# Kernel optimization log

Hardware: AMD Instinct MI355X
Metric: run time of the kernel (lower is better)

The kernel has to match this reference:

```python
import jax, jax.numpy as jnp
import numpy as np

M = 0.4        # margin
H = 0.333      # margin scaler slope
S = 64.0       # logit scale
BN_MEAN = 20.0     # running_mean of norm normalizer (affine=False, eval stats)
BN_VAR = 100.0 * 100.0
BN_EPS = 1e-3


def setup_inputs() -> dict:
    key = jax.random.key(0)
    k1, k2, k3 = jax.random.split(key, 3)
    embs = jax.random.normal(k1, (1024, 512), dtype=jnp.float32)
    weight = jax.random.normal(k2, (100000, 512), dtype=jnp.float32)
    labels = jax.random.randint(k3, (1024,), 0, 100000)
    return {"embs": embs, "weight": weight, "labels": labels}


def reference(embs, weight, labels):
    n = embs.shape[0]
    rows = jnp.arange(n)
    # feature norms and cosine logits
    norms = jnp.linalg.norm(embs, axis=1, keepdims=True)            # [N,1]
    w_norm = weight / jnp.linalg.norm(weight, axis=1, keepdims=True)  # [C,D]
    logits = (embs / norms) @ w_norm.T                               # [N,C]
    # norm-adaptive margin scaler (BatchNorm1d with running stats, affine=False)
    g = (norms[:, 0] - BN_MEAN) / jnp.sqrt(BN_VAR + BN_EPS)
    g = jnp.clip(g * H, -1.0, 1.0)                                   # [N]
    # angular margin at the label position
    theta = jnp.arccos(jnp.clip(logits.astype(jnp.float32), -0.999, 0.999))
    theta = theta.at[rows, labels].add(-M * g)
    logits_m = jnp.cos(jnp.clip(theta, 0.0, jnp.pi))
    # additive margin at the label position
    logits_m = logits_m.at[rows, labels].add(-(1.0 + M) * g)
    # scaled softmax cross-entropy (mean over batch)
    logp = jax.nn.log_softmax(logits_m * S, axis=-1)
    return -jnp.mean(logp[rows, labels])
```

## Files before the change

### kernel.cpp

```cpp
#include <hip/hip_runtime.h>
#include <math.h>

constexpr int N_ROWS = 1024;
constexpr int DDIM   = 512;
constexpr int C_CLS  = 100000;
constexpr float MARG = 0.4f;
constexpr int WPAD   = 100352;
constexpr int NT2    = 392;
constexpr int NT_FB  = 782;

typedef __attribute__((ext_vector_type(8))) short bf16x8;
typedef __attribute__((ext_vector_type(4))) float f32x4;
typedef __attribute__((address_space(1))) const void gvoid_t;
typedef __attribute__((address_space(3))) void lvoid_t;

__device__ __forceinline__ unsigned int f2bf(float x) {
    union { float f; unsigned int u; } v; v.f = x;
    return (v.u + 0x7FFFu + ((v.u >> 16) & 1u)) >> 16;
}

__device__ __forceinline__ float wave_sum(float s) {
    #pragma unroll
    for (int m = 1; m < 64; m <<= 1) s += __shfl_xor(s, m, 64);
    return s;
}

__global__ __launch_bounds__(256) void prep_embs(const float* __restrict__ embs,
                                                 float* __restrict__ g,
                                                 unsigned short* __restrict__ ehat) {
    const int row  = blockIdx.x * 4 + (threadIdx.x >> 6);
    const int lane = threadIdx.x & 63;
    const float4* src = (const float4*)(embs + (size_t)row * DDIM + lane * 8);
    const float4 a = src[0], b = src[1];
    float ss = a.x*a.x + a.y*a.y + a.z*a.z + a.w*a.w
             + b.x*b.x + b.y*b.y + b.z*b.z + b.w*b.w;
    ss = wave_sum(ss);
    const float norm = sqrtf(ss);
    const float rn = 1.f / norm;
    if (lane == 0) {
        float gg = (norm - 20.f) / sqrtf(10000.f + 1e-3f) * 0.333f;
        gg = fminf(fmaxf(gg, -1.f), 1.f);
        g[row] = gg;
    }
    uint4 pk;
    pk.x = f2bf(a.x*rn) | (f2bf(a.y*rn) << 16);
    pk.y = f2bf(a.z*rn) | (f2bf(a.w*rn) << 16);
    pk.z = f2bf(b.x*rn) | (f2bf(b.y*rn) << 16);
    pk.w = f2bf(b.z*rn) | (f2bf(b.w*rn) << 16);
    *(uint4*)(ehat + (size_t)row * DDIM + lane * 8) = pk;
}

__global__ __launch_bounds__(256) void prep_what(const float* __restrict__ w,
                                                 unsigned short* __restrict__ what) {
    const int row  = blockIdx.x * 4 + (threadIdx.x >> 6);
    const int lane = threadIdx.x & 63;
    const float4* src = (const float4*)(w + (size_t)row * DDIM + lane * 8);
    const float4 a = src[0], b = src[1];
    float ss = a.x*a.x + a.y*a.y + a.z*a.z + a.w*a.w
             + b.x*b.x + b.y*b.y + b.z*b.z + b.w*b.w;
    ss = wave_sum(ss);
    const float rn = rsqrtf(ss);
    uint4 pk;
    pk.x = f2bf(a.x*rn) | (f2bf(a.y*rn) << 16);
    pk.y = f2bf(a.z*rn) | (f2bf(a.w*rn) << 16);
    pk.z = f2bf(b.x*rn) | (f2bf(b.y*rn) << 16);
    pk.w = f2bf(b.z*rn) | (f2bf(b.w*rn) << 16);
    *(uint4*)(what + (size_t)row * DDIM + lane * 8) = pk;
}

__global__ __launch_bounds__(256) void prep_wnorm(const float* __restrict__ w,
                                                  float* __restrict__ rnormw) {
    const int row  = blockIdx.x * 4 + (threadIdx.x >> 6);
    const int lane = threadIdx.x & 63;
    const float4* src = (const float4*)(w + (size_t)row * DDIM + lane * 8);
    const float4 a = src[0], b = src[1];
    float ss = a.x*a.x + a.y*a.y + a.z*a.z + a.w*a.w
             + b.x*b.x + b.y*b.y + b.z*b.z + b.w*b.w;
    ss = wave_sum(ss);
    if (lane == 0) rnormw[row] = 1.f / sqrtf(ss);
}

__device__ __forceinline__ void stage_slab(const unsigned short* __restrict__ src,
                                           int grow0, const unsigned short* lds_row0,
                                           int kbase, int lane) {
    const int lr  = lane >> 3;
    const int c16 = (lane & 7) ^ lr;
    const unsigned short* g = src + (size_t)(grow0 + lr) * DDIM + kbase + c16 * 8;
    __builtin_amdgcn_global_load_lds((gvoid_t*)g, (lvoid_t*)lds_row0, 16, 0, 0);
}
__device__ __forceinline__ bf16x8 frag_ld(const unsigned short* tile, int row, int ks, int lane) {
    const int c16 = ((ks << 2) + (lane >> 4)) ^ (lane & 7);
    return *(const bf16x8*)(tile + row * 64 + c16 * 8);
}

__global__ __launch_bounds__(512, 2) void gemm256(
        const unsigned short* __restrict__ ehat,
        const unsigned short* __restrict__ what,
        const int* __restrict__ labels,
        float* __restrict__ psum,
        float* __restrict__ dlab)
{
    __shared__ __align__(16) unsigned short As[2][256 * 64];
    __shared__ __align__(16) unsigned short Bs[2][256 * 64];

    const int tid  = threadIdx.x;
    const int lane = tid & 63;
    const int wv   = tid >> 6;
    const int wr   = wv >> 2;
    const int wc   = wv & 3;

    const int nchunk = (int)gridDim.x >> 3;
    const int wgid   = ((int)blockIdx.x & 7) * nchunk + ((int)blockIdx.x >> 3);
    const int tile_c = wgid >> 2;
    const int tile_r = wgid & 3;
    const int row0   = tile_r * 256;
    const int col0   = tile_c * 256;

    f32x4 acc[8][4];
    #pragma unroll
    for (int m = 0; m < 8; ++m)
        #pragma unroll
        for (int n = 0; n < 4; ++n) acc[m][n] = f32x4{0.f, 0.f, 0.f, 0.f};

    #pragma unroll
    for (int s = 0; s < 8; ++s) {
        const int base = (s & 3) * 64 + wv * 8;
        if (s < 4) stage_slab(ehat, row0 + base, &As[0][base * 64], 0, lane);
        else       stage_slab(what, col0 + base, &Bs[0][base * 64], 0, lane);
    }
    asm volatile("s_waitcnt vmcnt(0)" ::: "memory");
    __builtin_amdgcn_s_barrier();

    for (int h = 0; h < 8; ++h) {
        const int cur = h & 1;
        const unsigned short* At = As[cur];
        const unsigned short* Bt = Bs[cur];
        const unsigned short* An = As[cur ^ 1];
        const unsigned short* Bn = Bs[cur ^ 1];
        const int kn = (h + 1) * 64;
        const bool do_stage = (h < 7);

        bf16x8 af[4][2], bf[4][2];

        #pragma unroll
        for (int q = 0; q < 4; ++q) {
            const int mh = q >> 1, nh = q & 1;
            if (q == 0 || q == 2) {
                #pragma unroll
                for (int m = 0; m < 4; ++m)
                    #pragma unroll
                    for (int ks = 0; ks < 2; ++ks)
                        af[m][ks] = frag_ld(At, wr * 128 + (mh * 4 + m) * 16 + (lane & 15), ks, lane);
            }
            if (q == 0 || q == 1) {
                #pragma unroll
                for (int n = 0; n < 2; ++n)
                    #pragma unroll
                    for (int ks = 0; ks < 2; ++ks)
                        bf[nh * 2 + n][ks] = frag_ld(Bt, wc * 64 + (nh * 2 + n) * 16 + (lane & 15), ks, lane);
            }
            if (do_stage) {
                #pragma unroll
                for (int s = 0; s < 8; ++s) {
                    const bool mine = (q == 0) ? (s < 3) : (q == 1) ? (s >= 3 && s < 6)
                                    : (q == 2) ? (s >= 6) : false;
                    if (mine) {
                        const int base = (s & 3) * 64 + wv * 8;
                        if (s < 4) stage_slab(ehat, row0 + base, &An[base * 64], kn, lane);
                        else       stage_slab(what, col0 + base, &Bn[base * 64], kn, lane);
                    }
                }
            }
            __builtin_amdgcn_s_barrier();
            asm volatile("s_waitcnt lgkmcnt(0)" ::: "memory");
            __builtin_amdgcn_s_setprio(1);
            #pragma unroll
            for (int m = 0; m < 4; ++m)
                #pragma unroll
                for (int n = 0; n < 2; ++n)
                    #pragma unroll
                    for (int ks = 0; ks < 2; ++ks)
                        acc[mh * 4 + m][nh * 2 + n] =
                            __builtin_amdgcn_mfma_f32_16x16x32_bf16(af[m][ks], bf[nh * 2 + n][ks],
                                                                    acc[mh * 4 + m][nh * 2 + n], 0, 0, 0);
            __builtin_amdgcn_s_setprio(0);
            if (q == 3) asm volatile("s_waitcnt vmcnt(0)" ::: "memory");
            __builtin_amdgcn_s_barrier();
        }
    }

    float* red = (float*)&As[0][0];
    #pragma unroll
    for (int m = 0; m < 8; ++m) {
        #pragma unroll
        for (int j = 0; j < 4; ++j) {
            const int lrow  = wr * 128 + m * 16 + ((lane >> 4) << 2) + j;
            const int r_abs = row0 + lrow;
            const int lab   = labels[r_abs];
            float s = 0.f;
            #pragma unroll
            for (int n = 0; n < 4; ++n) {
                const int c_abs = col0 + wc * 64 + n * 16 + (lane & 15);
                float v = acc[m][n][j];
                v = fminf(fmaxf(v, -0.999f), 0.999f);
                if (c_abs == lab) dlab[r_abs] = v;
                if (c_abs < C_CLS) s += __expf(64.f * v - 64.f);
            }
            #pragma unroll
            for (int msk = 1; msk < 16; msk <<= 1) s += __shfl_xor(s, msk, 64);
            if ((lane & 15) == 0) red[wc * 256 + lrow] = s;
        }
    }
    __syncthreads();
    for (int t = tid; t < 256; t += 512)
        psum[(size_t)(row0 + t) * NT2 + tile_c] = red[t] + red[256 + t] + red[512 + t] + red[768 + t];
}

__global__ __launch_bounds__(256, 2) void gemm_fused_fb(
        const unsigned short* __restrict__ ehat,
        const float* __restrict__ weight,
        const float* __restrict__ rnormw,
        const int* __restrict__ labels,
        float* __restrict__ psum,
        float* __restrict__ dlab)
{
    constexpr int BM = 128, BN = 128, BK = 32;
    __shared__ __align__(16) unsigned short Asf[BM * BK];
    __shared__ __align__(16) unsigned short Bsf[BN * BK];
    __shared__ float redbuf[2][BM];

    const int bid    = blockIdx.x;
    const int tile_c = bid >> 3;
    const int tile_r = bid & 7;
    const int row0   = tile_r * BM;
    const int col0   = tile_c * BN;

    const int tid  = threadIdx.x;
    const int lane = tid & 63;
    const int wv   = tid >> 6;
    const int wr   = wv >> 1;
    const int wc   = wv & 1;

    f32x4 acc[4][4];
    #pragma unroll
    for (int m = 0; m < 4; ++m)
        #pragma unroll
        for (int n = 0; n < 4; ++n) acc[m][n] = f32x4{0.f, 0.f, 0.f, 0.f};

    const int kq    = tid & 7;
    const int brow0 = tid >> 3;
    int   cidx[4];
    float rnv[4];
    #pragma unroll
    for (int p = 0; p < 4; ++p) {
        int c = col0 + p * 32 + brow0;
        c = c < C_CLS ? c : C_CLS - 1;
        cidx[p] = c;
        rnv[p]  = rnormw[c];
    }

    for (int kt = 0; kt < DDIM / BK; ++kt) {
        const int kbase = kt * BK;
        #pragma unroll
        for (int call = 0; call < 2; ++call) {
            const int chunk = call * 256 + tid;
            const uint4 d = *(const uint4*)(ehat + (size_t)(row0 + (chunk >> 2)) * DDIM
                                            + kbase + (chunk & 3) * 8);
            *(uint4*)(Asf + chunk * 8) = d;
        }
        #pragma unroll
        for (int p = 0; p < 4; ++p) {
            const float4 wd = *(const float4*)(weight + (size_t)cidx[p] * DDIM + kbase + kq * 4);
            const float r = rnv[p];
            const unsigned int lo = f2bf(wd.x * r) | (f2bf(wd.y * r) << 16);
            const unsigned int hi = f2bf(wd.z * r) | (f2bf(wd.w * r) << 16);
            *(uint2*)(Bsf + (p * 32 + brow0) * BK + kq * 4) = make_uint2(lo, hi);
        }
        __syncthreads();
        bf16x8 af[4], bfr[4];
        const int lr  = lane & 15;
        const int lko = (lane >> 4) * 8;
        #pragma unroll
        for (int m = 0; m < 4; ++m)
            af[m] = *(const bf16x8*)(Asf + (wr * 64 + m * 16 + lr) * BK + lko);
        #pragma unroll
        for (int n = 0; n < 4; ++n)
            bfr[n] = *(const bf16x8*)(Bsf + (wc * 64 + n * 16 + lr) * BK + lko);
        #pragma unroll
        for (int m = 0; m < 4; ++m)
            #pragma unroll
            for (int n = 0; n < 4; ++n)
                acc[m][n] = __builtin_amdgcn_mfma_f32_16x16x32_bf16(af[m], bfr[n], acc[m][n], 0, 0, 0);
        __syncthreads();
    }

    #pragma unroll
    for (int m = 0; m < 4; ++m) {
        #pragma unroll
        for (int j = 0; j < 4; ++j) {
            const int lrow  = wr * 64 + m * 16 + ((lane >> 4) << 2) + j;
            const int r_abs = row0 + lrow;
            const int lab   = labels[r_abs];
            float s = 0.f;
            #pragma unroll
            for (int n = 0; n < 4; ++n) {
                const int c_abs = col0 + wc * 64 + n * 16 + (lane & 15);
                float v = acc[m][n][j];
                v = fminf(fmaxf(v, -0.999f), 0.999f);
                if (c_abs == lab) dlab[r_abs] = v;
                if (c_abs < C_CLS) s += __expf(64.f * v - 64.f);
            }
            #pragma unroll
            for (int msk = 1; msk < 16; msk <<= 1) s += __shfl_xor(s, msk, 64);
            if ((lane & 15) == 0) redbuf[wc][lrow] = s;
        }
    }
    __syncthreads();
    for (int t = tid; t < BM; t += 256)
        psum[(size_t)(row0 + t) * NT_FB + tile_c] = redbuf[0][t] + redbuf[1][t];
}

__global__ __launch_bounds__(256) void reduce_rows(const float* __restrict__ psum,
                                                   const float* __restrict__ dlab,
                                                   const float* __restrict__ g,
                                                   float* __restrict__ losses, int nt) {
    const int row  = blockIdx.x * 4 + (threadIdx.x >> 6);
    const int lane = threadIdx.x & 63;
    const float* p = psum + (size_t)row * nt;
    float s = 0.f;
    for (int t = lane; t < nt; t += 64) s += p[t];
    s = wave_sum(s);
    if (lane == 0) {
        const float v  = dlab[row];
        const float gg = g[row];
        float th = acosf(v) - MARG * gg;
        th = fminf(fmaxf(th, 0.f), 3.14159265358979323846f);
        const float vm = cosf(th) - (1.f + MARG) * gg;
        s = s - __expf(64.f * v - 64.f) + __expf(64.f * vm - 64.f);
        losses[row] = 64.f + logf(s) - 64.f * vm;
    }
}

__global__ __launch_bounds__(256) void final_mean(const float* __restrict__ losses,
                                                  float* __restrict__ out) {
    const int tid = threadIdx.x;
    float s = 0.f;
    #pragma unroll
    for (int i = 0; i < 4; ++i) s += losses[tid + i * 256];
    s = wave_sum(s);
    __shared__ float red[4];
    if ((tid & 63) == 0) red[tid >> 6] = s;
    __syncthreads();
    if (tid == 0) out[0] = (red[0] + red[1] + red[2] + red[3]) * (1.f / 1024.f);
}

extern "C" void kernel_launch(void* const* d_in, const int* in_sizes, int n_in,
                              void* d_out, int out_size, void* d_ws, size_t ws_size,
                              hipStream_t stream) {
    const float* embs   = (const float*)d_in[0];
    const float* weight = (const float*)d_in[1];
    const int*   labels = (const int*)d_in[2];
    float* out = (float*)d_out;
    float* ws  = (float*)d_ws;

    const size_t WHAT_F = (size_t)WPAD * DDIM / 2;
    const size_t EHAT_F = (size_t)N_ROWS * DDIM / 2;
    const size_t PSUM_F = (size_t)N_ROWS * NT2;
    const size_t NEED_F = WHAT_F + EHAT_F + PSUM_F + 3 * 1024;

    if (ws_size >= NEED_F * sizeof(float)) {
        unsigned short* what = (unsigned short*)ws;
        unsigned short* ehat = (unsigned short*)(ws + WHAT_F);
        float* psum   = ws + WHAT_F + EHAT_F;
        float* gbuf   = psum + PSUM_F;
        float* dlab   = gbuf + 1024;
        float* losses = dlab + 1024;

        prep_embs<<<N_ROWS / 4, 256, 0, stream>>>(embs, gbuf, ehat);
        prep_what<<<C_CLS / 4, 256, 0, stream>>>(weight, what);
        gemm256<<<NT2 * 4, 512, 0, stream>>>(ehat, what, labels, psum, dlab);
        reduce_rows<<<N_ROWS / 4, 256, 0, stream>>>(psum, dlab, gbuf, losses, NT2);
        final_mean<<<1, 256, 0, stream>>>(losses, out);
    } else {
        float* rnormw = ws + 0;
        float* gbuf   = ws + 100352;
        float* dlab   = ws + 101376;
        float* losses = ws + 102400;
        unsigned short* ehat = (unsigned short*)(ws + 103424);
        float* psum   = ws + 103424 + 262144;

        prep_embs <<<N_ROWS / 4, 256, 0, stream>>>(embs, gbuf, ehat);
        prep_wnorm<<<C_CLS / 4, 256, 0, stream>>>(weight, rnormw);
        gemm_fused_fb<<<NT_FB * 8, 256, 0, stream>>>(ehat, weight, rnormw, labels, psum, dlab);
        reduce_rows<<<N_ROWS / 4, 256, 0, stream>>>(psum, dlab, gbuf, losses, NT_FB);
        final_mean<<<1, 256, 0, stream>>>(losses, out);
    }
}
```

Measured before the change: 222.6 us.

## Replace double-buffered K=64 GEMM pipeline with 4-slot K=32 ring prefetching three ahead

```diff
diff --git a/kernel.cpp b/kernel.cpp
--- a/kernel.cpp
+++ b/kernel.cpp
@@ -8,6 +8,7 @@
 constexpr int WPAD   = 100352;
 constexpr int NT2    = 392;
 constexpr int NT_FB  = 782;
+constexpr int TSLOT  = 256 * 32;
 
 typedef __attribute__((ext_vector_type(8))) short bf16x8;
 typedef __attribute__((ext_vector_type(4))) float f32x4;
@@ -80,28 +81,32 @@
     if (lane == 0) rnormw[row] = 1.f / sqrtf(ss);
 }
 
-__device__ __forceinline__ void stage_slab(const unsigned short* __restrict__ src,
-                                           int grow0, const unsigned short* lds_row0,
-                                           int kbase, int lane) {
-    const int lr  = lane >> 3;
-    const int c16 = (lane & 7) ^ lr;
-    const unsigned short* g = src + (size_t)(grow0 + lr) * DDIM + kbase + c16 * 8;
-    __builtin_amdgcn_global_load_lds((gvoid_t*)g, (lvoid_t*)lds_row0, 16, 0, 0);
-}
-__device__ __forceinline__ bf16x8 frag_ld(const unsigned short* tile, int row, int ks, int lane) {
-    const int c16 = ((ks << 2) + (lane >> 4)) ^ (lane & 7);
-    return *(const bf16x8*)(tile + row * 64 + c16 * 8);
-}
-
-__global__ __launch_bounds__(512, 2) void gemm256(
+__device__ __forceinline__ void stage_tile(const unsigned short* __restrict__ src,
+                                           int grow0, unsigned short* tile,
+                                           int kbase, int tid, int wv) {
+    #pragma unroll
+    for (int i = 0; i < 2; ++i) {
+        const int r  = i * 128 + (tid >> 2);
+        const int lc = (tid & 3) ^ ((r >> 1) & 3);
+        const unsigned short* g = src + (size_t)(grow0 + r) * DDIM + kbase + lc * 8;
+        __builtin_amdgcn_global_load_lds((gvoid_t*)g,
+            (lvoid_t*)(tile + i * 4096 + wv * 512), 16, 0, 0);
+    }
+}
+__device__ __forceinline__ bf16x8 frag32(const unsigned short* tile, int row, int lane) {
+    const int pc = (lane >> 4) ^ ((row >> 1) & 3);
+    return *(const bf16x8*)(tile + row * 32 + pc * 8);
+}
+
+__global__ __launch_bounds__(512, 2) void gemm256p(
         const unsigned short* __restrict__ ehat,
         const unsigned short* __restrict__ what,
         const int* __restrict__ labels,
         float* __restrict__ psum,
         float* __restrict__ dlab)
 {
-    __shared__ __align__(16) unsigned short As[2][256 * 64];
-    __shared__ __align__(16) unsigned short Bs[2][256 * 64];
+    __shared__ __align__(16) unsigned short Abuf[4 * TSLOT];
+    __shared__ __align__(16) unsigned short Bbuf[4 * TSLOT];
 
     const int tid  = threadIdx.x;
     const int lane = tid & 63;
@@ -123,73 +128,51 @@
         for (int n = 0; n < 4; ++n) acc[m][n] = f32x4{0.f, 0.f, 0.f, 0.f};
 
     #pragma unroll
-    for (int s = 0; s < 8; ++s) {
-        const int base = (s & 3) * 64 + wv * 8;
-        if (s < 4) stage_slab(ehat, row0 + base, &As[0][base * 64], 0, lane);
-        else       stage_slab(what, col0 + base, &Bs[0][base * 64], 0, lane);
-    }
+    for (int t = 0; t < 3; ++t) {
+        stage_tile(ehat, row0, Abuf + t * TSLOT, t * 32, tid, wv);
+        stage_tile(what, col0, Bbuf + t * TSLOT, t * 32, tid, wv);
+    }
+    asm volatile("s_waitcnt vmcnt(8)" ::: "memory");
+    __builtin_amdgcn_s_barrier();
+
+    auto body = [&](int h, bool do_stage) {
+        if (do_stage) {
+            const int hn = h + 3;
+            stage_tile(ehat, row0, Abuf + (hn & 3) * TSLOT, hn * 32, tid, wv);
+            stage_tile(what, col0, Bbuf + (hn & 3) * TSLOT, hn * 32, tid, wv);
+        }
+        const unsigned short* At = Abuf + (h & 3) * TSLOT;
+        const unsigned short* Bt = Bbuf + (h & 3) * TSLOT;
+        bf16x8 af[8], bf[4];
+        #pragma unroll
+        for (int m = 0; m < 8; ++m)
+            af[m] = frag32(At, wr * 128 + m * 16 + (lane & 15), lane);
+        #pragma unroll
+        for (int n = 0; n < 4; ++n)
+            bf[n] = frag32(Bt, wc * 64 + n * 16 + (lane & 15), lane);
+        __builtin_amdgcn_s_setprio(1);
+        #pragma unroll
+        for (int m = 0; m < 8; ++m)
+            #pragma unroll
+            for (int n = 0; n < 4; ++n)
+                acc[m][n] = __builtin_amdgcn_mfma_f32_16x16x32_bf16(af[m], bf[n], acc[m][n], 0, 0, 0);
+        __builtin_amdgcn_s_setprio(0);
+    };
+
+    for (int h = 0; h < 13; ++h) {
+        body(h, true);
+        asm volatile("s_waitcnt vmcnt(8)" ::: "memory");
+        __builtin_amdgcn_s_barrier();
+    }
+    body(13, false);
+    asm volatile("s_waitcnt vmcnt(4)" ::: "memory");
+    __builtin_amdgcn_s_barrier();
+    body(14, false);
     asm volatile("s_waitcnt vmcnt(0)" ::: "memory");
     __builtin_amdgcn_s_barrier();
-
-    for (int h = 0; h < 8; ++h) {
-        const int cur = h & 1;
-        const unsigned short* At = As[cur];
-        const unsigned short* Bt = Bs[cur];
-        const unsigned short* An = As[cur ^ 1];
-        const unsigned short* Bn = Bs[cur ^ 1];
-        const int kn = (h + 1) * 64;
-        const bool do_stage = (h < 7);
-
-        bf16x8 af[4][2], bf[4][2];
-
-        #pragma unroll
-        for (int q = 0; q < 4; ++q) {
-            const int mh = q >> 1, nh = q & 1;
-            if (q == 0 || q == 2) {
-                #pragma unroll
-                for (int m = 0; m < 4; ++m)
-                    #pragma unroll
-                    for (int ks = 0; ks < 2; ++ks)
-                        af[m][ks] = frag_ld(At, wr * 128 + (mh * 4 + m) * 16 + (lane & 15), ks, lane);
-            }
-            if (q == 0 || q == 1) {
-                #pragma unroll
-                for (int n = 0; n < 2; ++n)
-                    #pragma unroll
-                    for (int ks = 0; ks < 2; ++ks)
-                        bf[nh * 2 + n][ks] = frag_ld(Bt, wc * 64 + (nh * 2 + n) * 16 + (lane & 15), ks, lane);
-            }
-            if (do_stage) {
-                #pragma unroll
-                for (int s = 0; s < 8; ++s) {
-                    const bool mine = (q == 0) ? (s < 3) : (q == 1) ? (s >= 3 && s < 6)
-                                    : (q == 2) ? (s >= 6) : false;
-                    if (mine) {
-                        const int base = (s & 3) * 64 + wv * 8;
-                        if (s < 4) stage_slab(ehat, row0 + base, &An[base * 64], kn, lane);
-                        else       stage_slab(what, col0 + base, &Bn[base * 64], kn, lane);
-                    }
-                }
-            }
-            __builtin_amdgcn_s_barrier();
-            asm volatile("s_waitcnt lgkmcnt(0)" ::: "memory");
-            __builtin_amdgcn_s_setprio(1);
-            #pragma unroll
-            for (int m = 0; m < 4; ++m)
-                #pragma unroll
-                for (int n = 0; n < 2; ++n)
-                    #pragma unroll
-                    for (int ks = 0; ks < 2; ++ks)
-                        acc[mh * 4 + m][nh * 2 + n] =
-                            __builtin_amdgcn_mfma_f32_16x16x32_bf16(af[m][ks], bf[nh * 2 + n][ks],
-                                                                    acc[mh * 4 + m][nh * 2 + n], 0, 0, 0);
-            __builtin_amdgcn_s_setprio(0);
-            if (q == 3) asm volatile("s_waitcnt vmcnt(0)" ::: "memory");
-            __builtin_amdgcn_s_barrier();
-        }
-    }
-
-    float* red = (float*)&As[0][0];
+    body(15, false);
+
+    float* red = (float*)&Abuf[0];
     #pragma unroll
     for (int m = 0; m < 8; ++m) {
         #pragma unroll
@@ -378,7 +361,7 @@
 
         prep_embs<<<N_ROWS / 4, 256, 0, stream>>>(embs, gbuf, ehat);
         prep_what<<<C_CLS / 4, 256, 0, stream>>>(weight, what);
-        gemm256<<<NT2 * 4, 512, 0, stream>>>(ehat, what, labels, psum, dlab);
+        gemm256p<<<NT2 * 4, 512, 0, stream>>>(ehat, what, labels, psum, dlab);
         reduce_rows<<<N_ROWS / 4, 256, 0, stream>>>(psum, dlab, gbuf, losses, NT2);
         final_mean<<<1, 256, 0, stream>>>(losses, out);
     } else {
```

Result: no change. 222.6 us (+0.0%).

## Split LDS tiles into halves and prefetch halves across quadrant phases

Applied to the files above, without the earlier changes.

```diff
diff --git a/kernel.cpp b/kernel.cpp
--- a/kernel.cpp
+++ b/kernel.cpp
@@ -8,11 +8,14 @@
 constexpr int WPAD   = 100352;
 constexpr int NT2    = 392;
 constexpr int NT_FB  = 782;
+constexpr int TILE   = 256 * 64;
 
 typedef __attribute__((ext_vector_type(8))) short bf16x8;
 typedef __attribute__((ext_vector_type(4))) float f32x4;
 typedef __attribute__((address_space(1))) const void gvoid_t;
 typedef __attribute__((address_space(3))) void lvoid_t;
+
+#define WAITV(N) asm volatile("s_waitcnt vmcnt(" #N ")" ::: "memory")
 
 __device__ __forceinline__ unsigned int f2bf(float x) {
     union { float f; unsigned int u; } v; v.f = x;
@@ -80,34 +83,53 @@
     if (lane == 0) rnormw[row] = 1.f / sqrtf(ss);
 }
 
-__device__ __forceinline__ void stage_slab(const unsigned short* __restrict__ src,
-                                           int grow0, const unsigned short* lds_row0,
-                                           int kbase, int lane) {
-    const int lr  = lane >> 3;
-    const int c16 = (lane & 7) ^ lr;
-    const unsigned short* g = src + (size_t)(grow0 + lr) * DDIM + kbase + c16 * 8;
-    __builtin_amdgcn_global_load_lds((gvoid_t*)g, (lvoid_t*)lds_row0, 16, 0, 0);
-}
-__device__ __forceinline__ bf16x8 frag_ld(const unsigned short* tile, int row, int ks, int lane) {
-    const int c16 = ((ks << 2) + (lane >> 4)) ^ (lane & 7);
-    return *(const bf16x8*)(tile + row * 64 + c16 * 8);
-}
-
-__global__ __launch_bounds__(512, 2) void gemm256(
+__device__ __forceinline__ void stageA(const unsigned short* __restrict__ src, int grow0,
+                                       unsigned short* tile, int g, int kbase,
+                                       int wv, int lane) {
+    const int lr = lane >> 3;
+    const int lc = (lane & 7) ^ lr;
+    #pragma unroll
+    for (int i = 0; i < 2; ++i) {
+        const int s  = i * 8 + wv;
+        const int rb = ((s >> 3) << 7) | (g << 6) | ((s & 7) << 3);
+        const unsigned short* gp = src + (size_t)(grow0 + rb + lr) * DDIM + kbase + lc * 8;
+        __builtin_amdgcn_global_load_lds((gvoid_t*)gp, (lvoid_t*)(tile + rb * 64), 16, 0, 0);
+    }
+}
+__device__ __forceinline__ void stageB(const unsigned short* __restrict__ src, int grow0,
+                                       unsigned short* tile, int g, int kbase,
+                                       int wv, int lane) {
+    const int lr = lane >> 3;
+    const int lc = (lane & 7) ^ lr;
+    #pragma unroll
+    for (int i = 0; i < 2; ++i) {
+        const int s  = i * 8 + wv;
+        const int rb = ((s >> 2) << 6) | (g << 5) | ((s & 3) << 3);
+        const unsigned short* gp = src + (size_t)(grow0 + rb + lr) * DDIM + kbase + lc * 8;
+        __builtin_amdgcn_global_load_lds((gvoid_t*)gp, (lvoid_t*)(tile + rb * 64), 16, 0, 0);
+    }
+}
+__device__ __forceinline__ bf16x8 frag64(const unsigned short* tile, int row, int ks, int lane) {
+    const int pc = ((ks << 2) + (lane >> 4)) ^ (lane & 7);
+    return *(const bf16x8*)(tile + row * 64 + pc * 8);
+}
+
+__global__ __launch_bounds__(512, 2) void gemm256q(
         const unsigned short* __restrict__ ehat,
         const unsigned short* __restrict__ what,
         const int* __restrict__ labels,
         float* __restrict__ psum,
         float* __restrict__ dlab)
 {
-    __shared__ __align__(16) unsigned short As[2][256 * 64];
-    __shared__ __align__(16) unsigned short Bs[2][256 * 64];
+    __shared__ __align__(16) unsigned short Abuf[2 * TILE];
+    __shared__ __align__(16) unsigned short Bbuf[2 * TILE];
 
     const int tid  = threadIdx.x;
     const int lane = tid & 63;
     const int wv   = tid >> 6;
     const int wr   = wv >> 2;
     const int wc   = wv & 3;
+    const int lr15 = lane & 15;
 
     const int nchunk = (int)gridDim.x >> 3;
     const int wgid   = ((int)blockIdx.x & 7) * nchunk + ((int)blockIdx.x >> 3);
@@ -122,74 +144,108 @@
         #pragma unroll
         for (int n = 0; n < 4; ++n) acc[m][n] = f32x4{0.f, 0.f, 0.f, 0.f};
 
-    #pragma unroll
-    for (int s = 0; s < 8; ++s) {
-        const int base = (s & 3) * 64 + wv * 8;
-        if (s < 4) stage_slab(ehat, row0 + base, &As[0][base * 64], 0, lane);
-        else       stage_slab(what, col0 + base, &Bs[0][base * 64], 0, lane);
-    }
-    asm volatile("s_waitcnt vmcnt(0)" ::: "memory");
+    stageA(ehat, row0, Abuf, 0, 0, wv, lane);
+    stageB(what, col0, Bbuf, 0, 0, wv, lane);
+    stageA(ehat, row0, Abuf, 1, 0, wv, lane);
+    stageB(what, col0, Bbuf, 1, 0, wv, lane);
+    stageA(ehat, row0, Abuf + TILE, 0, 64, wv, lane);
+    stageB(what, col0, Bbuf + TILE, 0, 64, wv, lane);
+    WAITV(8);
     __builtin_amdgcn_s_barrier();
 
-    for (int h = 0; h < 8; ++h) {
-        const int cur = h & 1;
-        const unsigned short* At = As[cur];
-        const unsigned short* Bt = Bs[cur];
-        const unsigned short* An = As[cur ^ 1];
-        const unsigned short* Bn = Bs[cur ^ 1];
-        const int kn = (h + 1) * 64;
-        const bool do_stage = (h < 7);
-
-        bf16x8 af[4][2], bf[4][2];
-
-        #pragma unroll
-        for (int q = 0; q < 4; ++q) {
-            const int mh = q >> 1, nh = q & 1;
-            if (q == 0 || q == 2) {
+    for (int t = 0; t < 8; ++t) {
+        unsigned short* curA = Abuf + (t & 1) * TILE;
+        unsigned short* curB = Bbuf + (t & 1) * TILE;
+        unsigned short* nxtA = Abuf + ((t & 1) ^ 1) * TILE;
+        unsigned short* nxtB = Bbuf + ((t & 1) ^ 1) * TILE;
+        bf16x8 af[4][2], bfv[2][2][2];
+
+        #pragma unroll
+        for (int m = 0; m < 4; ++m)
+            #pragma unroll
+            for (int ks = 0; ks < 2; ++ks)
+                af[m][ks] = frag64(curA, wr * 128 + m * 16 + lr15, ks, lane);
+        #pragma unroll
+        for (int n = 0; n < 2; ++n)
+            #pragma unroll
+            for (int ks = 0; ks < 2; ++ks)
+                bfv[0][n][ks] = frag64(curB, wc * 64 + n * 16 + lr15, ks, lane);
+        if (t < 7) stageA(ehat, row0, nxtA, 1, (t + 1) * 64, wv, lane);
+        __builtin_amdgcn_sched_barrier(0);
+        __builtin_amdgcn_s_barrier();
+        asm volatile("s_waitcnt lgkmcnt(0)" ::: "memory");
+        __builtin_amdgcn_sched_barrier(0);
+        __builtin_amdgcn_s_setprio(1);
+        #pragma unroll
+        for (int m = 0; m < 4; ++m)
+            #pragma unroll
+            for (int n = 0; n < 2; ++n)
                 #pragma unroll
-                for (int m = 0; m < 4; ++m)
-                    #pragma unroll
-                    for (int ks = 0; ks < 2; ++ks)
-                        af[m][ks] = frag_ld(At, wr * 128 + (mh * 4 + m) * 16 + (lane & 15), ks, lane);
-            }
-            if (q == 0 || q == 1) {
+                for (int ks = 0; ks < 2; ++ks)
+                    acc[m][n] = __builtin_amdgcn_mfma_f32_16x16x32_bf16(af[m][ks], bfv[0][n][ks], acc[m][n], 0, 0, 0);
+        __builtin_amdgcn_s_setprio(0);
+        if (t < 7) { WAITV(6); } else { WAITV(0); }
+        __builtin_amdgcn_s_barrier();
+
+        #pragma unroll
+        for (int n = 0; n < 2; ++n)
+            #pragma unroll
+            for (int ks = 0; ks < 2; ++ks)
+                bfv[1][n][ks] = frag64(curB, wc * 64 + 32 + n * 16 + lr15, ks, lane);
+        if (t < 7) stageB(what, col0, nxtB, 1, (t + 1) * 64, wv, lane);
+        __builtin_amdgcn_sched_barrier(0);
+        __builtin_amdgcn_s_barrier();
+        asm volatile("s_waitcnt lgkmcnt(0)" ::: "memory");
+        __builtin_amdgcn_sched_barrier(0);
+        __builtin_amdgcn_s_setprio(1);
+        #pragma unroll
+        for (int m = 0; m < 4; ++m)
+            #pragma unroll
+            for (int n = 0; n < 2; ++n)
                 #pragma unroll
-                for (int n = 0; n < 2; ++n)
-                    #pragma unroll
-                    for (int ks = 0; ks < 2; ++ks)
-                        bf[nh * 2 + n][ks] = frag_ld(Bt, wc * 64 + (nh * 2 + n) * 16 + (lane & 15), ks, lane);
-            }
-            if (do_stage) {
+                for (int ks = 0; ks < 2; ++ks)
+                    acc[m][2 + n] = __builtin_amdgcn_mfma_f32_16x16x32_bf16(af[m][ks], bfv[1][n][ks], acc[m][2 + n], 0, 0, 0);
+        __builtin_amdgcn_s_setprio(0);
+        __builtin_amdgcn_s_barrier();
+
+        #pragma unroll
+        for (int m = 0; m < 4; ++m)
+            #pragma unroll
+            for (int ks = 0; ks < 2; ++ks)
+                af[m][ks] = frag64(curA, wr * 128 + 64 + m * 16 + lr15, ks, lane);
+        if (t < 6) stageA(ehat, row0, curA, 0, (t + 2) * 64, wv, lane);
+        __builtin_amdgcn_sched_barrier(0);
+        __builtin_amdgcn_s_barrier();
+        asm volatile("s_waitcnt lgkmcnt(0)" ::: "memory");
+        __builtin_amdgcn_sched_barrier(0);
+        __builtin_amdgcn_s_setprio(1);
+        #pragma unroll
+        for (int m = 0; m < 4; ++m)
+            #pragma unroll
+            for (int n = 0; n < 2; ++n)
                 #pragma unroll
-                for (int s = 0; s < 8; ++s) {
-                    const bool mine = (q == 0) ? (s < 3) : (q == 1) ? (s >= 3 && s < 6)
-                                    : (q == 2) ? (s >= 6) : false;
-                    if (mine) {
-                        const int base = (s & 3) * 64 + wv * 8;
-                        if (s < 4) stage_slab(ehat, row0 + base, &An[base * 64], kn, lane);
-                        else       stage_slab(what, col0 + base, &Bn[base * 64], kn, lane);
-                    }
-                }
-            }
-            __builtin_amdgcn_s_barrier();
-            asm volatile("s_waitcnt lgkmcnt(0)" ::: "memory");
-            __builtin_amdgcn_s_setprio(1);
-            #pragma unroll
-            for (int m = 0; m < 4; ++m)
+                for (int ks = 0; ks < 2; ++ks)
+                    acc[4 + m][n] = __builtin_amdgcn_mfma_f32_16x16x32_bf16(af[m][ks], bfv[0][n][ks], acc[4 + m][n], 0, 0, 0);
+        __builtin_amdgcn_s_setprio(0);
+        __builtin_amdgcn_s_barrier();
+
+        if (t < 6) stageB(what, col0, curB, 0, (t + 2) * 64, wv, lane);
+        __builtin_amdgcn_sched_barrier(0);
+        __builtin_amdgcn_s_barrier();
+        __builtin_amdgcn_s_setprio(1);
+        #pragma unroll
+        for (int m = 0; m < 4; ++m)
+            #pragma unroll
+            for (int n = 0; n < 2; ++n)
                 #pragma unroll
-                for (int n = 0; n < 2; ++n)
-                    #pragma unroll
-                    for (int ks = 0; ks < 2; ++ks)
-                        acc[mh * 4 + m][nh * 2 + n] =
-                            __builtin_amdgcn_mfma_f32_16x16x32_bf16(af[m][ks], bf[nh * 2 + n][ks],
-                                                                    acc[mh * 4 + m][nh * 2 + n], 0, 0, 0);
-            __builtin_amdgcn_s_setprio(0);
-            if (q == 3) asm volatile("s_waitcnt vmcnt(0)" ::: "memory");
-            __builtin_amdgcn_s_barrier();
-        }
-    }
-
-    float* red = (float*)&As[0][0];
+                for (int ks = 0; ks < 2; ++ks)
+                    acc[4 + m][2 + n] = __builtin_amdgcn_mfma_f32_16x16x32_bf16(af[m][ks], bfv[1][n][ks], acc[4 + m][2 + n], 0, 0, 0);
+        __builtin_amdgcn_s_setprio(0);
+        if (t < 6) { WAITV(8); } else if (t == 6) { WAITV(4); } else { WAITV(0); }
+        __builtin_amdgcn_s_barrier();
+    }
+
+    float* red = (float*)&Abuf[0];
     #pragma unroll
     for (int m = 0; m < 8; ++m) {
         #pragma unroll
@@ -378,7 +434,7 @@
 
         prep_embs<<<N_ROWS / 4, 256, 0, stream>>>(embs, gbuf, ehat);
         prep_what<<<C_CLS / 4, 256, 0, stream>>>(weight, what);
-        gemm256<<<NT2 * 4, 512, 0, stream>>>(ehat, what, labels, psum, dlab);
+        gemm256q<<<NT2 * 4, 512, 0, stream>>>(ehat, what, labels, psum, dlab);
         reduce_rows<<<N_ROWS / 4, 256, 0, stream>>>(psum, dlab, gbuf, losses, NT2);
         final_mean<<<1, 256, 0, stream>>>(losses, out);
     } else {
```

Result: no change. 221.7 us (-0.4%).
